# Optimization experiments

Hardware: AMD Instinct MI355X
Metric: run time of the kernel (lower is better)

Reference implementation:

```python
import jax, jax.numpy as jnp
import numpy as np

# Grid / physics constants (match init_kwargs)
NX, NY, NZ = 256, 256, 128
LX, LY, LZ = 1.0, 1.0, 1.0
CP, CV, MU, KTH, G = 1004.0, 717.0, 1.8e-5, 0.025, 9.8
DX = LX / NX            # periodic spacing in x
DY = LY / NY            # periodic spacing in y
DZ = LZ / (NZ - 1)      # non-periodic spacing in z


def _d1p(f, axis, d):
    # second-order central first derivative, periodic axis
    return (jnp.roll(f, -1, axis) - jnp.roll(f, 1, axis)) * (0.5 / d)


def _d2p(f, axis, d):
    # second-order central second derivative, periodic axis
    return (jnp.roll(f, -1, axis) + jnp.roll(f, 1, axis) - 2.0 * f) * (1.0 / (d * d))


def _d1z(f, d):
    # non-periodic first derivative along last axis: central interior, 2nd-order one-sided at walls
    inv2d = 0.5 / d
    c = (f[..., 2:] - f[..., :-2]) * inv2d
    lo = (-3.0 * f[..., 0:1] + 4.0 * f[..., 1:2] - f[..., 2:3]) * inv2d
    hi = (3.0 * f[..., -1:] - 4.0 * f[..., -2:-1] + f[..., -3:-2]) * inv2d
    return jnp.concatenate([lo, c, hi], axis=-1)


def _d2z(f, d):
    # non-periodic second derivative along last axis: central interior, 2nd-order one-sided at walls
    invd2 = 1.0 / (d * d)
    c = (f[..., 2:] - 2.0 * f[..., 1:-1] + f[..., :-2]) * invd2
    lo = (2.0 * f[..., 0:1] - 5.0 * f[..., 1:2] + 4.0 * f[..., 2:3] - f[..., 3:4]) * invd2
    hi = (2.0 * f[..., -1:] - 5.0 * f[..., -2:-1] + 4.0 * f[..., -3:-2] - f[..., -4:-3]) * invd2
    return jnp.concatenate([lo, c, hi], axis=-1)


def _lap(f):
    return _d2p(f, 0, DX) + _d2p(f, 1, DY) + _d2z(f, DZ)


def _adv(q, u, v, w):
    # u*dq/dx + v*dq/dy + w*dq/dz
    return u * _d1p(q, 0, DX) + v * _d1p(q, 1, DY) + w * _d1z(q, DZ)


def setup_inputs() -> dict:
    key = jax.random.key(0)
    state = 0.05 * jax.random.normal(key, (6, NX, NY, NZ), dtype=jnp.float32)
    # keep density positive and temperature physical (state order: u,v,w,rou,T,c)
    state = state.at[3].add(1.0)
    state = state.at[4].add(300.0)
    return {"state": state, "t": 0}


def reference(state, t):
    u, v, w, rou, T, c = state  # each [NX, NY, NZ]
    p = (CP - CV) * rou * T

    # NOTE: original code only applies -d/dx(rou*u) to drou; the y/z flux line is a no-op expression.
    drou = -_d1p(rou * u, 0, DX)

    du = (-_d1p(p, 0, DX) + MU * _lap(u)) / rou - _adv(u, u, v, w)
    dv = (-_d1p(p, 1, DY) + MU * _lap(v)) / rou - _adv(v, u, v, w)
    dw = (-G * rou - _d1z(p, DZ) + MU * _lap(w)) / rou - _adv(w, u, v, w)
    dT = KTH * _lap(T) / rou / CV - _adv(T, u, v, w)
    dc = -_adv(c, u, v, w)

    result = jnp.stack([du, dv, dw, drou, dT, dc], axis=0)
    # zero momentum and temperature tendencies at z walls
    result = result.at[0:3, :, :, 0].set(0.0)
    result = result.at[0:3, :, :, -1].set(0.0)
    result = result.at[4, :, :, 0].set(0.0)
    result = result.at[4, :, :, -1].set(0.0)
    return result
```

## Files before the change

### kernel.cpp

```cpp
#include <hip/hip_runtime.h>


namespace {
constexpr int NXc = 256, NYc = 256, NZc = 128;
constexpr int FS = NXc * NYc * NZc;
constexpr int XS = NYc * NZc;
constexpr int YS = NZc;

constexpr float MUc = 1.8e-5f, KTHc = 0.025f, Gc = 9.8f;
constexpr float Rgas = 287.0f;
constexpr float invCV = 1.0f / 717.0f;

constexpr float inv2dx = 128.0f, inv2dy = 128.0f, inv2dz = 63.5f;
constexpr float invdx2 = 65536.0f, invdy2 = 65536.0f, invdz2 = 16129.0f;
}

__device__ __forceinline__ float4 ld4(const float* __restrict__ p, int i4) {
    return reinterpret_cast<const float4*>(p)[i4];
}

#define LOADN(q, sq) \
    const float4 q##_xm = ld4(sq, bxm4), q##_xp = ld4(sq, bxp4); \
    const float4 q##_ym = ld4(sq, bym4), q##_yp = ld4(sq, byp4); \
    const float q##_zm = __shfl_up(q##_c.w, 1, 32); \
    const float q##_zp = __shfl_down(q##_c.x, 1, 32);

#define ADV_LAP_C(q, C, PREV, NEXT) \
    adv_##q.C = u_c.C * (q##_xp.C - q##_xm.C) * inv2dx \
              + v_c.C * (q##_yp.C - q##_ym.C) * inv2dy \
              + w_c.C * ((NEXT) - (PREV)) * inv2dz; \
    lap_##q.C = (q##_xp.C + q##_xm.C - 2.0f * q##_c.C) * invdx2 \
              + (q##_yp.C + q##_ym.C - 2.0f * q##_c.C) * invdy2 \
              + ((NEXT) + (PREV) - 2.0f * q##_c.C) * invdz2;

#define DERIVS(q) \
    float4 adv_##q, lap_##q; \
    ADV_LAP_C(q, x, q##_zm,  q##_c.y) \
    ADV_LAP_C(q, y, q##_c.x, q##_c.z) \
    ADV_LAP_C(q, z, q##_c.y, q##_c.w) \
    ADV_LAP_C(q, w, q##_c.z, q##_zp)

__global__ __launch_bounds__(256) void rb_kernel(const float* __restrict__ s,
                                                 float* __restrict__ o) {
    const int l = threadIdx.x;
    const int y = blockIdx.x * 8 + threadIdx.y;
    const int x = blockIdx.y;

    const int xm = (x == 0) ? NXc - 1 : x - 1;
    const int xp = (x == NXc - 1) ? 0 : x + 1;
    const int ym = (y == 0) ? NYc - 1 : y - 1;
    const int yp = (y == NYc - 1) ? 0 : y + 1;

    const int b4   = (x * XS + y * YS) / 4 + l;
    const int bxm4 = (xm * XS + y * YS) / 4 + l;
    const int bxp4 = (xp * XS + y * YS) / 4 + l;
    const int bym4 = (x * XS + ym * YS) / 4 + l;
    const int byp4 = (x * XS + yp * YS) / 4 + l;

    const float* su = s;
    const float* sv = s + FS;
    const float* sw = s + 2 * FS;
    const float* sr = s + 3 * FS;
    const float* st = s + 4 * FS;
    const float* sc = s + 5 * FS;

    const float4 u_c = ld4(su, b4), v_c = ld4(sv, b4), w_c = ld4(sw, b4);
    const float4 r_c = ld4(sr, b4), T_c = ld4(st, b4), c_c = ld4(sc, b4);

    float4 inv_r;
    inv_r.x = 1.0f / r_c.x; inv_r.y = 1.0f / r_c.y;
    inv_r.z = 1.0f / r_c.z; inv_r.w = 1.0f / r_c.w;

    LOADN(T, st)
    DERIVS(T)
    LOADN(r, sr)

    float4 p_c, p_xm, p_xp, p_ym, p_yp;
#define PC(C) \
    p_c.C  = Rgas * r_c.C  * T_c.C; \
    p_xm.C = Rgas * r_xm.C * T_xm.C;  p_xp.C = Rgas * r_xp.C * T_xp.C; \
    p_ym.C = Rgas * r_ym.C * T_ym.C;  p_yp.C = Rgas * r_yp.C * T_yp.C;
    PC(x) PC(y) PC(z) PC(w)
#undef PC
    const float p_zm = __shfl_up(p_c.w, 1, 32);
    const float p_zp = __shfl_down(p_c.x, 1, 32);

    float4 dpdx, dpdy, dpdz;
#define DP(C) \
    dpdx.C = (p_xp.C - p_xm.C) * inv2dx; \
    dpdy.C = (p_yp.C - p_ym.C) * inv2dy;
    DP(x) DP(y) DP(z) DP(w)
#undef DP
    dpdz.x = (p_c.y - p_zm) * inv2dz;
    dpdz.y = (p_c.z - p_c.x) * inv2dz;
    dpdz.z = (p_c.w - p_c.y) * inv2dz;
    dpdz.w = (p_zp  - p_c.z) * inv2dz;

    LOADN(u, su)
    DERIVS(u)
    float4 drou;
#define DR(C) drou.C = -(r_xp.C * u_xp.C - r_xm.C * u_xm.C) * inv2dx;
    DR(x) DR(y) DR(z) DR(w)
#undef DR

    LOADN(v, sv)
    DERIVS(v)

    LOADN(w, sw)
    DERIVS(w)

    LOADN(c, sc)
    DERIVS(c)
    (void)lap_c;

    float4 du4, dv4, dw4, dT4, dc4;
#define OUT(C) \
    du4.C = (-dpdx.C + MUc * lap_u.C) * inv_r.C - adv_u.C; \
    dv4.C = (-dpdy.C + MUc * lap_v.C) * inv_r.C - adv_v.C; \
    dw4.C = (-Gc * r_c.C - dpdz.C + MUc * lap_w.C) * inv_r.C - adv_w.C; \
    dT4.C = KTHc * lap_T.C * inv_r.C * invCV - adv_T.C; \
    dc4.C = -adv_c.C;
    OUT(x) OUT(y) OUT(z) OUT(w)
#undef OUT

    if (l == 0) {
        du4.x = 0.0f; dv4.x = 0.0f; dw4.x = 0.0f; dT4.x = 0.0f;
        const float dzc0 = (-3.0f * c_c.x + 4.0f * c_c.y - c_c.z) * inv2dz;
        dc4.x = -(u_c.x * (c_xp.x - c_xm.x) * inv2dx
                + v_c.x * (c_yp.x - c_ym.x) * inv2dy
                + w_c.x * dzc0);
    }
    if (l == 31) {
        du4.w = 0.0f; dv4.w = 0.0f; dw4.w = 0.0f; dT4.w = 0.0f;
        const float dzcN = (3.0f * c_c.w - 4.0f * c_c.z + c_c.y) * inv2dz;
        dc4.w = -(u_c.w * (c_xp.w - c_xm.w) * inv2dx
                + v_c.w * (c_yp.w - c_ym.w) * inv2dy
                + w_c.w * dzcN);
    }

    float4* o4 = reinterpret_cast<float4*>(o);
    const int fs4 = FS / 4;
    o4[b4]           = du4;
    o4[b4 + fs4]     = dv4;
    o4[b4 + 2 * fs4] = dw4;
    o4[b4 + 3 * fs4] = drou;
    o4[b4 + 4 * fs4] = dT4;
    o4[b4 + 5 * fs4] = dc4;
}

extern "C" void kernel_launch(void* const* d_in, const int* in_sizes, int n_in,
                              void* d_out, int out_size, void* d_ws, size_t ws_size,
                              hipStream_t stream) {
    (void)in_sizes; (void)n_in; (void)d_ws; (void)ws_size; (void)out_size;
    const float* s = (const float*)d_in[0];
    float* o = (float*)d_out;

    dim3 block(32, 8, 1);
    dim3 grid(NYc / 8, NXc, 1);
    rb_kernel<<<grid, block, 0, stream>>>(s, o);
}
```

Measured before the change: 347.5 us.

## Use nontemporal stores, store each output early, and cap registers via launch bounds

Each output field is now computed and written inside its own scope right after its neighbor loads, which shortens live ranges so fewer registers are held at once. The output writes use nontemporal stores so they do not pollute cache needed for the stencil neighbor reads. Launch bounds now request 4 blocks per CU to push for higher occupancy, at the risk of spilling if register pressure stays high.

```diff
diff --git a/kernel.cpp b/kernel.cpp
--- a/kernel.cpp
+++ b/kernel.cpp
@@ -13,10 +13,18 @@
 
 constexpr float inv2dx = 128.0f, inv2dy = 128.0f, inv2dz = 63.5f;
 constexpr float invdx2 = 65536.0f, invdy2 = 65536.0f, invdz2 = 16129.0f;
+
+typedef float nf4 __attribute__((ext_vector_type(4)));
 }
 
 __device__ __forceinline__ float4 ld4(const float* __restrict__ p, int i4) {
     return reinterpret_cast<const float4*>(p)[i4];
+}
+
+__device__ __forceinline__ void st_nt(float4 v, float4* p) {
+    nf4 nv;
+    nv.x = v.x; nv.y = v.y; nv.z = v.z; nv.w = v.w;
+    __builtin_nontemporal_store(nv, reinterpret_cast<nf4*>(p));
 }
 
 #define LOADN(q, sq) \
@@ -40,8 +48,8 @@
     ADV_LAP_C(q, z, q##_c.y, q##_c.w) \
     ADV_LAP_C(q, w, q##_c.z, q##_zp)
 
-__global__ __launch_bounds__(256) void rb_kernel(const float* __restrict__ s,
-                                                 float* __restrict__ o) {
+__global__ __launch_bounds__(256, 4) void rb_kernel(const float* __restrict__ s,
+                                                    float* __restrict__ o) {
     const int l = threadIdx.x;
     const int y = blockIdx.x * 8 + threadIdx.y;
     const int x = blockIdx.y;
@@ -64,6 +72,9 @@
     const float* st = s + 4 * FS;
     const float* sc = s + 5 * FS;
 
+    float4* o4 = reinterpret_cast<float4*>(o);
+    const int fs4 = FS / 4;
+
     const float4 u_c = ld4(su, b4), v_c = ld4(sv, b4), w_c = ld4(sw, b4);
     const float4 r_c = ld4(sr, b4), T_c = ld4(st, b4), c_c = ld4(sc, b4);
 
@@ -72,7 +83,6 @@
     inv_r.z = 1.0f / r_c.z; inv_r.w = 1.0f / r_c.w;
 
     LOADN(T, st)
-    DERIVS(T)
     LOADN(r, sr)
 
     float4 p_c, p_xm, p_xp, p_ym, p_yp;
@@ -96,56 +106,85 @@
     dpdz.z = (p_c.w - p_c.y) * inv2dz;
     dpdz.w = (p_zp  - p_c.z) * inv2dz;
 
-    LOADN(u, su)
-    DERIVS(u)
-    float4 drou;
-#define DR(C) drou.C = -(r_xp.C * u_xp.C - r_xm.C * u_xm.C) * inv2dx;
-    DR(x) DR(y) DR(z) DR(w)
-#undef DR
-
-    LOADN(v, sv)
-    DERIVS(v)
-
-    LOADN(w, sw)
-    DERIVS(w)
-
-    LOADN(c, sc)
-    DERIVS(c)
-    (void)lap_c;
-
-    float4 du4, dv4, dw4, dT4, dc4;
-#define OUT(C) \
-    du4.C = (-dpdx.C + MUc * lap_u.C) * inv_r.C - adv_u.C; \
-    dv4.C = (-dpdy.C + MUc * lap_v.C) * inv_r.C - adv_v.C; \
-    dw4.C = (-Gc * r_c.C - dpdz.C + MUc * lap_w.C) * inv_r.C - adv_w.C; \
-    dT4.C = KTHc * lap_T.C * inv_r.C * invCV - adv_T.C; \
-    dc4.C = -adv_c.C;
-    OUT(x) OUT(y) OUT(z) OUT(w)
-#undef OUT
-
-    if (l == 0) {
-        du4.x = 0.0f; dv4.x = 0.0f; dw4.x = 0.0f; dT4.x = 0.0f;
-        const float dzc0 = (-3.0f * c_c.x + 4.0f * c_c.y - c_c.z) * inv2dz;
-        dc4.x = -(u_c.x * (c_xp.x - c_xm.x) * inv2dx
-                + v_c.x * (c_yp.x - c_ym.x) * inv2dy
-                + w_c.x * dzc0);
-    }
-    if (l == 31) {
-        du4.w = 0.0f; dv4.w = 0.0f; dw4.w = 0.0f; dT4.w = 0.0f;
-        const float dzcN = (3.0f * c_c.w - 4.0f * c_c.z + c_c.y) * inv2dz;
-        dc4.w = -(u_c.w * (c_xp.w - c_xm.w) * inv2dx
-                + v_c.w * (c_yp.w - c_ym.w) * inv2dy
-                + w_c.w * dzcN);
-    }
-
-    float4* o4 = reinterpret_cast<float4*>(o);
-    const int fs4 = FS / 4;
-    o4[b4]           = du4;
-    o4[b4 + fs4]     = dv4;
-    o4[b4 + 2 * fs4] = dw4;
-    o4[b4 + 3 * fs4] = drou;
-    o4[b4 + 4 * fs4] = dT4;
-    o4[b4 + 5 * fs4] = dc4;
+    {
+        DERIVS(T)
+        float4 dT4;
+        dT4.x = KTHc * lap_T.x * inv_r.x * invCV - adv_T.x;
+        dT4.y = KTHc * lap_T.y * inv_r.y * invCV - adv_T.y;
+        dT4.z = KTHc * lap_T.z * inv_r.z * invCV - adv_T.z;
+        dT4.w = KTHc * lap_T.w * inv_r.w * invCV - adv_T.w;
+        if (l == 0)  dT4.x = 0.0f;
+        if (l == 31) dT4.w = 0.0f;
+        st_nt(dT4, o4 + b4 + 4 * fs4);
+    }
+
+    {
+        LOADN(u, su)
+        DERIVS(u)
+        float4 du4, drou;
+#define OUTU(C) \
+        du4.C  = (-dpdx.C + MUc * lap_u.C) * inv_r.C - adv_u.C; \
+        drou.C = -(r_xp.C * u_xp.C - r_xm.C * u_xm.C) * inv2dx;
+        OUTU(x) OUTU(y) OUTU(z) OUTU(w)
+#undef OUTU
+        if (l == 0)  du4.x = 0.0f;
+        if (l == 31) du4.w = 0.0f;
+        st_nt(du4,  o4 + b4);
+        st_nt(drou, o4 + b4 + 3 * fs4);
+    }
+
+    {
+        LOADN(v, sv)
+        DERIVS(v)
+        float4 dv4;
+        dv4.x = (-dpdy.x + MUc * lap_v.x) * inv_r.x - adv_v.x;
+        dv4.y = (-dpdy.y + MUc * lap_v.y) * inv_r.y - adv_v.y;
+        dv4.z = (-dpdy.z + MUc * lap_v.z) * inv_r.z - adv_v.z;
+        dv4.w = (-dpdy.w + MUc * lap_v.w) * inv_r.w - adv_v.w;
+        if (l == 0)  dv4.x = 0.0f;
+        if (l == 31) dv4.w = 0.0f;
+        st_nt(dv4, o4 + b4 + fs4);
+    }
+
+    {
+        LOADN(w, sw)
+        DERIVS(w)
+        float4 dw4;
+        dw4.x = (-Gc * r_c.x - dpdz.x + MUc * lap_w.x) * inv_r.x - adv_w.x;
+        dw4.y = (-Gc * r_c.y - dpdz.y + MUc * lap_w.y) * inv_r.y - adv_w.y;
+        dw4.z = (-Gc * r_c.z - dpdz.z + MUc * lap_w.z) * inv_r.z - adv_w.z;
+        dw4.w = (-Gc * r_c.w - dpdz.w + MUc * lap_w.w) * inv_r.w - adv_w.w;
+        if (l == 0)  dw4.x = 0.0f;
+        if (l == 31) dw4.w = 0.0f;
+        st_nt(dw4, o4 + b4 + 2 * fs4);
+    }
+
+    {
+        LOADN(c, sc)
+        float4 dc4;
+#define DC(C, PREV, NEXT) \
+        dc4.C = -(u_c.C * (c_xp.C - c_xm.C) * inv2dx \
+                + v_c.C * (c_yp.C - c_ym.C) * inv2dy \
+                + w_c.C * ((NEXT) - (PREV)) * inv2dz);
+        DC(x, c_zm,  c_c.y)
+        DC(y, c_c.x, c_c.z)
+        DC(z, c_c.y, c_c.w)
+        DC(w, c_c.z, c_zp)
+#undef DC
+        if (l == 0) {
+            const float dzc0 = (-3.0f * c_c.x + 4.0f * c_c.y - c_c.z) * inv2dz;
+            dc4.x = -(u_c.x * (c_xp.x - c_xm.x) * inv2dx
+                    + v_c.x * (c_yp.x - c_ym.x) * inv2dy
+                    + w_c.x * dzc0);
+        }
+        if (l == 31) {
+            const float dzcN = (3.0f * c_c.w - 4.0f * c_c.z + c_c.y) * inv2dz;
+            dc4.w = -(u_c.w * (c_xp.w - c_xm.w) * inv2dx
+                    + v_c.w * (c_yp.w - c_ym.w) * inv2dy
+                    + w_c.w * dzcN);
+        }
+        st_nt(dc4, o4 + b4 + 5 * fs4);
+    }
 }
 
 extern "C" void kernel_launch(void* const* d_in, const int* in_sizes, int n_in,
```

Measured after the change: 350.9 us. Within noise of the previous version (+1.0%).
